# Kernel tuning notes

Hardware: AMD Instinct MI355X
Metric: run time of the kernel (lower is better)

Reference implementation:

```python
import jax
import jax.numpy as jnp
from jax import lax
import numpy as np

E = 4          # num_experts
CIN = 128
COUT = 128
K = 3
STAT = 6
HID = 16       # router hidden width
STRIDE = 1
PAD = 1


def setup_inputs() -> dict:
    key = jax.random.key(0)
    ks = jax.random.split(key, 8)
    B, H, W = 32, 64, 64
    x = jax.random.normal(ks[0], (B, CIN, H, W), dtype=jnp.float32)
    scene_stats = jax.random.normal(ks[1], (B, STAT), dtype=jnp.float32)
    # router: Linear(stat_dim,16) -> ReLU -> Linear(16,E) -> Softmax
    W1 = jax.random.normal(ks[2], (HID, STAT), dtype=jnp.float32) * (1.0 / np.sqrt(STAT))
    b1 = jnp.zeros((HID,), dtype=jnp.float32)
    W2 = jax.random.normal(ks[3], (E, HID), dtype=jnp.float32) * (1.0 / np.sqrt(HID))
    b2 = jnp.zeros((E,), dtype=jnp.float32)
    weight_experts = jax.random.normal(ks[4], (E, COUT, CIN, K, K), dtype=jnp.float32) * 0.02
    bias_experts = jnp.zeros((E, COUT), dtype=jnp.float32)
    return {"x": x, "scene_stats": scene_stats, "W1": W1, "b1": b1,
            "W2": W2, "b2": b2, "weight_experts": weight_experts,
            "bias_experts": bias_experts}


def reference(x, scene_stats, W1, b1, W2, b2, weight_experts, bias_experts):
    B, Cin, H, W = x.shape
    Cout = weight_experts.shape[1]
    # router
    h = jax.nn.relu(scene_stats @ W1.T + b1)                 # [B, HID]
    routing = jax.nn.softmax(h @ W2.T + b2, axis=1)          # [B, E]
    # per-sample dynamic weights / bias
    dyn_w = jnp.einsum('bk,koihw->boihw', routing, weight_experts)  # [B,Cout,Cin,K,K]
    dyn_b = jnp.einsum('bk,ko->bo', routing, bias_experts)          # [B,Cout]
    # grouped conv with groups = B (each sample uses its own filter bank)
    x_r = x.reshape(1, B * Cin, H, W)
    w_r = dyn_w.reshape(B * Cout, Cin, K, K)
    out = lax.conv_general_dilated(
        x_r, w_r,
        window_strides=(STRIDE, STRIDE),
        padding=((PAD, PAD), (PAD, PAD)),
        feature_group_count=B,
        dimension_numbers=('NCHW', 'OIHW', 'NCHW'))
    out = out.reshape(B, Cout, out.shape[2], out.shape[3])
    return out + dyn_b[:, :, None, None]
```

## Files before the change

kernel.cpp:

```cpp
#include <hip/hip_runtime.h>
#include <hip/hip_bf16.h>


typedef short bf16x8 __attribute__((ext_vector_type(8)));
typedef float f32x4  __attribute__((ext_vector_type(4)));

#define VMWAIT(n) asm volatile("s_waitcnt vmcnt(" #n ")" ::: "memory")
#define LGKM0()   asm volatile("s_waitcnt lgkmcnt(0)" ::: "memory")

static __device__ __forceinline__ unsigned short f2bf(float f) {
    unsigned u = __float_as_uint(f);
    u = u + 0x7FFFu + ((u >> 16) & 1u);
    return (unsigned short)(u >> 16);
}

static __device__ __forceinline__ void gl2lds16(const unsigned short* g, unsigned short* l) {
    __builtin_amdgcn_global_load_lds(
        (const __attribute__((address_space(1))) unsigned int*)g,
        (__attribute__((address_space(3))) unsigned int*)l,
        16, 0, 0);
}

__global__ void prep_kernel(const float* __restrict__ stats, const float* __restrict__ W1,
                            const float* __restrict__ b1, const float* __restrict__ W2,
                            const float* __restrict__ b2, const float* __restrict__ wexp,
                            const float* __restrict__ bexp, unsigned short* __restrict__ dynw,
                            float* __restrict__ dynb)
{
    __shared__ float ls[4*1152];
    __shared__ float lr[32*4];
    const int tid = threadIdx.x;
    const int co  = blockIdx.x & 127;
    const int bg  = blockIdx.x >> 7;

    if (tid < 32) {
        float s[6];
#pragma unroll
        for (int i = 0; i < 6; ++i) s[i] = stats[tid*6 + i];
        float h[16];
#pragma unroll
        for (int j = 0; j < 16; ++j) {
            float a = b1[j];
#pragma unroll
            for (int i = 0; i < 6; ++i) a += W1[j*6+i]*s[i];
            h[j] = a > 0.f ? a : 0.f;
        }
        float lg[4];
#pragma unroll
        for (int e = 0; e < 4; ++e) {
            float a = b2[e];
#pragma unroll
            for (int j = 0; j < 16; ++j) a += W2[e*16+j]*h[j];
            lg[e] = a;
        }
        float m = fmaxf(fmaxf(lg[0],lg[1]), fmaxf(lg[2],lg[3]));
        float ex[4], sum = 0.f;
#pragma unroll
        for (int e = 0; e < 4; ++e) { ex[e] = expf(lg[e]-m); sum += ex[e]; }
        float inv = 1.f / sum;
#pragma unroll
        for (int e = 0; e < 4; ++e) lr[tid*4+e] = ex[e]*inv;
    }
    for (int i = tid; i < 4*1152; i += 256) {
        int e = i / 1152, j = i - e*1152;
        ls[i] = wexp[((unsigned long long)(e*128 + co))*1152 + j];
    }
    __syncthreads();

    if (bg == 0 && tid < 32) {
        float sb = 0.f;
#pragma unroll
        for (int e = 0; e < 4; ++e) sb += lr[tid*4+e] * bexp[e*128 + co];
        dynb[tid*128 + co] = sb;
    }

    const int ci  = tid & 127;
    const int tp0 = tid >> 7;
    const int cic = ci >> 5;
    const int g   = (ci >> 3) & 3;
    const int jj  = ci & 7;
    const int mi  = co >> 4;
    const int l15 = co & 15;
    for (int bb = bg*8; bb < bg*8 + 8; ++bb) {
        float r0 = lr[bb*4+0], r1 = lr[bb*4+1], r2 = lr[bb*4+2], r3 = lr[bb*4+3];
#pragma unroll
        for (int pp = 0; pp < 5; ++pp) {
            int tap = 2*pp + tp0;
            if (tap < 9) {
                int j = ci*9 + tap;
                float v = r0*ls[j] + r1*ls[1152+j] + r2*ls[2*1152+j] + r3*ls[3*1152+j];
                dynw[((((unsigned long long)(bb*4 + cic)*9 + tap)*8 + mi)*64 + g*16 + l15)*8 + jj] = f2bf(v);
            }
        }
    }
}

__global__ __launch_bounds__(256, 2) void conv_kernel(
    const float* __restrict__ x,
    const unsigned short* __restrict__ dynw,
    const float* __restrict__ dynb,
    float* __restrict__ out)
{
    __shared__ __align__(16) unsigned short xs[6*66*32];
    __shared__ __align__(16) unsigned short wsm[6][4096];

    const int tid  = threadIdx.x;
    const int wave = tid >> 6;
    const int lane = tid & 63;
    const int l15  = lane & 15;
    const int g    = lane >> 4;
    const int pr    = tid >> 4;
    const int c4    = tid & 15;
    const int p2col = tid & 63;
    const int p2cg  = tid >> 6;

    int bidx = ((blockIdx.x & 7) << 6) | (blockIdx.x >> 3);
    const int b  = bidx >> 4;
    const int r0 = (bidx & 15) << 2;

    f32x4 acc[8][4];
#pragma unroll
    for (int mi = 0; mi < 8; ++mi)
#pragma unroll
        for (int ni = 0; ni < 4; ++ni) acc[mi][ni] = (f32x4){0.f,0.f,0.f,0.f};

    const float* xsrcb = x + (unsigned long long)b*(128ull*64*64);
    const unsigned short* wsrcb = dynw + (unsigned long long)b*(4ull*9*4096);

#define P1ISSUE(kk)                                                            \
    do {                                                                       \
        int grow_ = r0 + (kk) - 1;                                             \
        int growc_ = grow_ < 0 ? 0 : (grow_ > 63 ? 63 : grow_);                \
        const float* xp_ = xsrcb + (unsigned)((cic_*32 + 2*pr)*4096)           \
                         + growc_*64 + c4*4;                                   \
        xv[(kk)%3][0] = *(const float4*)xp_;                                   \
        xv[(kk)%3][1] = *(const float4*)(xp_ + 4096);                          \
    } while (0)

#define P1PROC(kk)                                                             \
    do {                                                                       \
        int grow_ = r0 + (kk) - 1;                                             \
        bool oob_ = (grow_ < 0) || (grow_ > 63);                               \
        float4 va_ = xv[(kk)%3][0], vb_ = xv[(kk)%3][1];                       \
        unsigned w0_ = oob_ ? 0u : (f2bf(va_.x) | ((unsigned)f2bf(vb_.x) << 16)); \
        unsigned w1_ = oob_ ? 0u : (f2bf(va_.y) | ((unsigned)f2bf(vb_.y) << 16)); \
        unsigned w2_ = oob_ ? 0u : (f2bf(va_.z) | ((unsigned)f2bf(vb_.z) << 16)); \
        unsigned w3_ = oob_ ? 0u : (f2bf(va_.w) | ((unsigned)f2bf(vb_.w) << 16)); \
        *(uint4*)((char*)xs + (kk)*4224 + pr*256 + c4*16)                      \
            = make_uint4(w0_, w1_, w2_, w3_);                                  \
    } while (0)

#define XSTAGE2(CIC_, WFIRST_)                                                 \
    do {                                                                       \
        const int cic_ = (CIC_);                                               \
        _Pragma("unroll")                                                      \
        for (int t = 0; t < 3; ++t) {                                          \
            const unsigned short* wsrc_ = wsrcb + (unsigned)(((WFIRST_) + t)*4096); \
            unsigned short* wd_ = wsm[((WFIRST_) + t) % 6];                    \
            gl2lds16(wsrc_ + (unsigned)tid*8,       wd_ + (unsigned)tid*8);    \
            gl2lds16(wsrc_ + (unsigned)(tid+256)*8, wd_ + (unsigned)(tid+256)*8); \
        }                                                                      \
        {                                                                      \
            float4 xv[3][2];                                                   \
            P1ISSUE(0); P1ISSUE(1); P1ISSUE(2);                                \
            VMWAIT(4); P1PROC(0); P1ISSUE(3);                                  \
            VMWAIT(4); P1PROC(1); P1ISSUE(4);                                  \
            VMWAIT(4); P1PROC(2); P1ISSUE(5);                                  \
            VMWAIT(4); P1PROC(3);                                              \
            VMWAIT(2); P1PROC(4);                                              \
            VMWAIT(0); P1PROC(5);                                              \
        }                                                                      \
        LGKM0();                                                               \
        __builtin_amdgcn_s_barrier();                                          \
        __builtin_amdgcn_sched_barrier(0);                                     \
        _Pragma("unroll")                                                      \
        for (int h = 0; h < 2; ++h) {                                          \
            uint4 tv[3];                                                       \
            _Pragma("unroll")                                                  \
            for (int r = 0; r < 3; ++r) {                                      \
                const char* rb_ = (const char*)xs + (h*3 + r)*4224             \
                                + p2cg*1024 + p2col*4;                         \
                tv[r].x = *(const unsigned*)(rb_);                             \
                tv[r].y = *(const unsigned*)(rb_ + 256);                       \
                tv[r].z = *(const unsigned*)(rb_ + 512);                       \
                tv[r].w = *(const unsigned*)(rb_ + 768);                       \
            }                                                                  \
            LGKM0();                                                           \
            __builtin_amdgcn_s_barrier();                                      \
            __builtin_amdgcn_sched_barrier(0);                                 \
            int lcol_ = p2col + 1;                                             \
            int wb_   = ((p2cg + (lcol_ >> 1)) & 3) << 4;                      \
            _Pragma("unroll")                                                  \
            for (int r = 0; r < 3; ++r)                                        \
                *(uint4*)((char*)xs + (h*3 + r)*4224 + lcol_*64 + wb_) = tv[r];\
        }                                                                      \
        if (tid < 24)                                                          \
            *(uint4*)((char*)xs + (tid>>2)*4224 + (tid&3)*16)                  \
                = make_uint4(0,0,0,0);                                         \
        LGKM0();                                                               \
        __builtin_amdgcn_s_barrier();                                          \
        __builtin_amdgcn_sched_barrier(0);                                     \
    } while (0)

    if (tid < 24)
        *(uint4*)((char*)xs + (tid>>2)*4224 + 65*64 + (tid&3)*16) = make_uint4(0,0,0,0);
    XSTAGE2(0, 0);

#pragma unroll
    for (int p = 0; p < 12; ++p) {
        const int cic = p / 3;
        if (p > 0) {
            VMWAIT(0);
            __builtin_amdgcn_s_barrier();
            __builtin_amdgcn_sched_barrier(0);
        }
        if ((p % 3) == 0 && p > 0) {
            XSTAGE2(cic, 3*p + 3);
        } else if (p < 11) {
#pragma unroll
            for (int t = 0; t < 3; ++t) {
                const int s = 3*p + 3 + t;
                const unsigned short* wsrc = wsrcb + (unsigned)(s*4096);
                unsigned short* wd = wsm[s % 6];
                gl2lds16(wsrc + (unsigned)tid*8,       wd + (unsigned)tid*8);
                gl2lds16(wsrc + (unsigned)(tid+256)*8, wd + (unsigned)(tid+256)*8);
            }
        }
        const int ky   = p % 3;
        const int lrow = wave + ky;
        __builtin_amdgcn_s_setprio(1);
#pragma unroll
        for (int kx = 0; kx < 3; ++kx) {
            const unsigned short* wb = wsm[(3*p + kx) % 6];
            bf16x8 afrag[8];
#pragma unroll
            for (int mi = 0; mi < 8; ++mi)
                afrag[mi] = *(const bf16x8*)(wb + (unsigned)((mi*64 + lane)*8));
#pragma unroll
            for (int ni = 0; ni < 4; ++ni) {
                int lcol = 16*ni + l15 + kx;
                int boff = (lrow*66 + lcol)*64 + (((g + (lcol >> 1)) & 3) << 4);
                bf16x8 bfrag = *(const bf16x8*)((const char*)xs + boff);
#pragma unroll
                for (int mi = 0; mi < 8; ++mi)
                    acc[mi][ni] = __builtin_amdgcn_mfma_f32_16x16x32_bf16(
                                      afrag[mi], bfrag, acc[mi][ni], 0, 0, 0);
            }
        }
        __builtin_amdgcn_s_setprio(0);
    }

    const int y = r0 + wave;
#pragma unroll
    for (int mi = 0; mi < 8; ++mi) {
#pragma unroll
        for (int r = 0; r < 4; ++r) {
            int co = 16*mi + g*4 + r;
            float bias = dynb[b*128 + co];
            float* op = out + (((unsigned long long)(b*128 + co))*64 + y)*64;
#pragma unroll
            for (int ni = 0; ni < 4; ++ni)
                op[16*ni + l15] = acc[mi][ni][r] + bias;
        }
    }
#undef XSTAGE2
#undef P1PROC
#undef P1ISSUE
}

extern "C" void kernel_launch(void* const* d_in, const int* in_sizes, int n_in,
                              void* d_out, int out_size, void* d_ws, size_t ws_size,
                              hipStream_t stream)
{
    const float* x     = (const float*)d_in[0];
    const float* stats = (const float*)d_in[1];
    const float* W1    = (const float*)d_in[2];
    const float* b1    = (const float*)d_in[3];
    const float* W2    = (const float*)d_in[4];
    const float* b2    = (const float*)d_in[5];
    const float* wexp  = (const float*)d_in[6];
    const float* bexp  = (const float*)d_in[7];
    float* out = (float*)d_out;

    char* ws = (char*)d_ws;
    float* dynb           = (float*)(ws + 512);
    unsigned short* dynw  = (unsigned short*)(ws + 32768);

    prep_kernel<<<512, 256, 0, stream>>>(stats, W1, b1, W2, b2, wexp, bexp, dynw, dynb);
    conv_kernel<<<512, 256, 0, stream>>>(x, dynw, dynb, out);
}
```

Before: 65.51 us.

## Drop LDS transpose pass; gather B fragments from channel-pair-major padded layout

Removes the second staging phase that re-read the input tile from LDS and wrote it back transposed into a swizzled column-major layout, along with its two extra barriers per stage. The input tile now stays channel-pair-major with a padded row stride (272 bytes), and each MFMA B fragment is assembled from four 4-byte LDS reads instead of one 16-byte read. Left padding maps to a zeroed spare column. The global prefetch depth for x is also cut from three rows to two. In exchange, the inner MFMA loop issues four times as many LDS read instructions per B fragment.

```diff
diff --git a/kernel.cpp b/kernel.cpp
--- a/kernel.cpp
+++ b/kernel.cpp
@@ -4,6 +4,7 @@
 
 typedef short bf16x8 __attribute__((ext_vector_type(8)));
 typedef float f32x4  __attribute__((ext_vector_type(4)));
+typedef unsigned u32x4 __attribute__((ext_vector_type(4)));
 
 #define VMWAIT(n) asm volatile("s_waitcnt vmcnt(" #n ")" ::: "memory")
 #define LGKM0()   asm volatile("s_waitcnt lgkmcnt(0)" ::: "memory")
@@ -101,7 +102,7 @@
     const float* __restrict__ dynb,
     float* __restrict__ out)
 {
-    __shared__ __align__(16) unsigned short xs[6*66*32];
+    __shared__ __align__(16) unsigned short xs[6*16*136];
     __shared__ __align__(16) unsigned short wsm[6][4096];
 
     const int tid  = threadIdx.x;
@@ -109,10 +110,8 @@
     const int lane = tid & 63;
     const int l15  = lane & 15;
     const int g    = lane >> 4;
-    const int pr    = tid >> 4;
-    const int c4    = tid & 15;
-    const int p2col = tid & 63;
-    const int p2cg  = tid >> 6;
+    const int pr   = tid >> 4;
+    const int c4   = tid & 15;
 
     int bidx = ((blockIdx.x & 7) << 6) | (blockIdx.x >> 3);
     const int b  = bidx >> 4;
@@ -133,24 +132,24 @@
         int growc_ = grow_ < 0 ? 0 : (grow_ > 63 ? 63 : grow_);                \
         const float* xp_ = xsrcb + (unsigned)((cic_*32 + 2*pr)*4096)           \
                          + growc_*64 + c4*4;                                   \
-        xv[(kk)%3][0] = *(const float4*)xp_;                                   \
-        xv[(kk)%3][1] = *(const float4*)(xp_ + 4096);                          \
+        xv[(kk)&1][0] = *(const float4*)xp_;                                   \
+        xv[(kk)&1][1] = *(const float4*)(xp_ + 4096);                          \
     } while (0)
 
 #define P1PROC(kk)                                                             \
     do {                                                                       \
         int grow_ = r0 + (kk) - 1;                                             \
         bool oob_ = (grow_ < 0) || (grow_ > 63);                               \
-        float4 va_ = xv[(kk)%3][0], vb_ = xv[(kk)%3][1];                       \
+        float4 va_ = xv[(kk)&1][0], vb_ = xv[(kk)&1][1];                       \
         unsigned w0_ = oob_ ? 0u : (f2bf(va_.x) | ((unsigned)f2bf(vb_.x) << 16)); \
         unsigned w1_ = oob_ ? 0u : (f2bf(va_.y) | ((unsigned)f2bf(vb_.y) << 16)); \
         unsigned w2_ = oob_ ? 0u : (f2bf(va_.z) | ((unsigned)f2bf(vb_.z) << 16)); \
         unsigned w3_ = oob_ ? 0u : (f2bf(va_.w) | ((unsigned)f2bf(vb_.w) << 16)); \
-        *(uint4*)((char*)xs + (kk)*4224 + pr*256 + c4*16)                      \
+        *(uint4*)((char*)xs + (kk)*4352 + pr*272 + c4*16)                      \
             = make_uint4(w0_, w1_, w2_, w3_);                                  \
     } while (0)
 
-#define XSTAGE2(CIC_, WFIRST_)                                                 \
+#define XSTAGE(CIC_, WFIRST_)                                                  \
     do {                                                                       \
         const int cic_ = (CIC_);                                               \
         _Pragma("unroll")                                                      \
@@ -161,50 +160,24 @@
             gl2lds16(wsrc_ + (unsigned)(tid+256)*8, wd_ + (unsigned)(tid+256)*8); \
         }                                                                      \
         {                                                                      \
-            float4 xv[3][2];                                                   \
-            P1ISSUE(0); P1ISSUE(1); P1ISSUE(2);                                \
-            VMWAIT(4); P1PROC(0); P1ISSUE(3);                                  \
-            VMWAIT(4); P1PROC(1); P1ISSUE(4);                                  \
-            VMWAIT(4); P1PROC(2); P1ISSUE(5);                                  \
-            VMWAIT(4); P1PROC(3);                                              \
+            float4 xv[2][2];                                                   \
+            P1ISSUE(0); P1ISSUE(1);                                            \
+            VMWAIT(2); P1PROC(0); P1ISSUE(2);                                  \
+            VMWAIT(2); P1PROC(1); P1ISSUE(3);                                  \
+            VMWAIT(2); P1PROC(2); P1ISSUE(4);                                  \
+            VMWAIT(2); P1PROC(3); P1ISSUE(5);                                  \
             VMWAIT(2); P1PROC(4);                                              \
             VMWAIT(0); P1PROC(5);                                              \
         }                                                                      \
         LGKM0();                                                               \
         __builtin_amdgcn_s_barrier();                                          \
         __builtin_amdgcn_sched_barrier(0);                                     \
-        _Pragma("unroll")                                                      \
-        for (int h = 0; h < 2; ++h) {                                          \
-            uint4 tv[3];                                                       \
-            _Pragma("unroll")                                                  \
-            for (int r = 0; r < 3; ++r) {                                      \
-                const char* rb_ = (const char*)xs + (h*3 + r)*4224             \
-                                + p2cg*1024 + p2col*4;                         \
-                tv[r].x = *(const unsigned*)(rb_);                             \
-                tv[r].y = *(const unsigned*)(rb_ + 256);                       \
-                tv[r].z = *(const unsigned*)(rb_ + 512);                       \
-                tv[r].w = *(const unsigned*)(rb_ + 768);                       \
-            }                                                                  \
-            LGKM0();                                                           \
-            __builtin_amdgcn_s_barrier();                                      \
-            __builtin_amdgcn_sched_barrier(0);                                 \
-            int lcol_ = p2col + 1;                                             \
-            int wb_   = ((p2cg + (lcol_ >> 1)) & 3) << 4;                      \
-            _Pragma("unroll")                                                  \
-            for (int r = 0; r < 3; ++r)                                        \
-                *(uint4*)((char*)xs + (h*3 + r)*4224 + lcol_*64 + wb_) = tv[r];\
-        }                                                                      \
-        if (tid < 24)                                                          \
-            *(uint4*)((char*)xs + (tid>>2)*4224 + (tid&3)*16)                  \
-                = make_uint4(0,0,0,0);                                         \
-        LGKM0();                                                               \
-        __builtin_amdgcn_s_barrier();                                          \
-        __builtin_amdgcn_sched_barrier(0);                                     \
     } while (0)
 
-    if (tid < 24)
-        *(uint4*)((char*)xs + (tid>>2)*4224 + 65*64 + (tid&3)*16) = make_uint4(0,0,0,0);
-    XSTAGE2(0, 0);
+    if (tid < 96)
+        *(uint4*)((char*)xs + (tid >> 4)*4352 + (tid & 15)*272 + 256)
+            = make_uint4(0,0,0,0);
+    XSTAGE(0, 0);
 
 #pragma unroll
     for (int p = 0; p < 12; ++p) {
@@ -215,7 +188,7 @@
             __builtin_amdgcn_sched_barrier(0);
         }
         if ((p % 3) == 0 && p > 0) {
-            XSTAGE2(cic, 3*p + 3);
+            XSTAGE(cic, 3*p + 3);
         } else if (p < 11) {
 #pragma unroll
             for (int t = 0; t < 3; ++t) {
@@ -238,9 +211,15 @@
                 afrag[mi] = *(const bf16x8*)(wb + (unsigned)((mi*64 + lane)*8));
 #pragma unroll
             for (int ni = 0; ni < 4; ++ni) {
-                int lcol = 16*ni + l15 + kx;
-                int boff = (lrow*66 + lcol)*64 + (((g + (lcol >> 1)) & 3) << 4);
-                bf16x8 bfrag = *(const bf16x8*)((const char*)xs + boff);
+                int c = 16*ni + l15 + kx - 1;
+                int w = (c < 0) ? 65 : c;
+                const char* bp = (const char*)xs + lrow*4352 + g*1088 + w*4;
+                u32x4 bv;
+                bv.x = *(const unsigned*)(bp);
+                bv.y = *(const unsigned*)(bp + 272);
+                bv.z = *(const unsigned*)(bp + 544);
+                bv.w = *(const unsigned*)(bp + 816);
+                bf16x8 bfrag = __builtin_bit_cast(bf16x8, bv);
 #pragma unroll
                 for (int mi = 0; mi < 8; ++mi)
                     acc[mi][ni] = __builtin_amdgcn_mfma_f32_16x16x32_bf16(
@@ -263,7 +242,7 @@
                 op[16*ni + l15] = acc[mi][ni][r] + bias;
         }
     }
-#undef XSTAGE2
+#undef XSTAGE
 #undef P1PROC
 #undef P1ISSUE
 }
```

New measurement: 60.26 us. 1.09x faster.
